# Kernel optimization log

Hardware: AMD Instinct MI355X
Metric: run time of the kernel (lower is better)

Reference implementation:

```python
import jax, jax.numpy as jnp
import numpy as np

N, CIN, T = 10000, 64, 64
COUT, K = 64, 3


def setup_inputs() -> dict:
    key = jax.random.key(0)
    k1, k2, k3 = jax.random.split(key, 3)
    x = jax.random.normal(k1, (N, CIN, T), dtype=jnp.float32)
    # torch Conv1d default init: uniform(-1/sqrt(fan_in), 1/sqrt(fan_in))
    bound = 1.0 / np.sqrt(CIN * K)
    weight = jax.random.uniform(k2, (2 * COUT, CIN, K), dtype=jnp.float32, minval=-bound, maxval=bound)
    bias = jax.random.uniform(k3, (2 * COUT,), dtype=jnp.float32, minval=-bound, maxval=bound)
    return {"x": x, "weight": weight, "bias": bias}


def reference(x, weight, bias):
    # Batched 1D conv over time for all nodes at once (equivalent to the
    # per-node loop in the original, since weights are shared).
    # x: [N, Cin, T], weight: [2*Cout, Cin, K] -> y: [N, 2*Cout, T-K+1]
    y = jax.lax.conv_general_dilated(
        x, weight, window_strides=(1,), padding="VALID",
        dimension_numbers=("NCH", "OIH", "NCH"))
    y = y + bias[None, :, None]
    # GLU along channel dim: first half gated by sigmoid of second half
    a, b = jnp.split(y, 2, axis=1)
    return a * jax.nn.sigmoid(b)
```

## Files before the change

kernel.cpp:

```cpp
#include <hip/hip_runtime.h>
#include <hip/hip_bf16.h>

typedef __attribute__((ext_vector_type(8))) short short8;
typedef __attribute__((ext_vector_type(4))) float float4v;

#define NSAMP 10000
#define CIN   64
#define TLEN  64
#define COUT  64
#define TOUT  62

static __device__ __forceinline__ ushort f2bf(float v) {
    unsigned int x = __float_as_uint(v);
    return (ushort)((x + 0x7fffu + ((x >> 16) & 1u)) >> 16);
}

__global__ void prep_weights(const float* __restrict__ w, ushort* __restrict__ wa) {
    int o = blockIdx.x * blockDim.x + threadIdx.x;
    if (o >= 128 * 192) return;
    int co = o / 192;
    int kk = o - co * 192;
    int k  = kk >> 6;
    int ci = kk & 63;
    wa[o] = f2bf(w[co * 192 + ci * 3 + k]);
}

__global__ __launch_bounds__(256, 2)
void conv_glu(const float* __restrict__ x, const ushort* __restrict__ wa,
              const float* __restrict__ bias, float* __restrict__ out) {
    const int n   = blockIdx.x;
    const int tid = threadIdx.x;
    const int w   = tid >> 6;
    const int L   = tid & 63;
    const int l   = L & 15;
    const int q   = L >> 4;
    const int h   = w & 1;
    const int nh  = w >> 1;
    const int t0base = nh * 32;

    const float* xs = x + n * (CIN * TLEN);

    short8 afr[4][6];
#pragma unroll
    for (int mt = 0; mt < 4; ++mt) {
        int co = 32 * h + 16 * (mt & 1) + 64 * (mt >> 1) + l;
        const short8* wrow = (const short8*)(wa + co * 192);
#pragma unroll
        for (int kc = 0; kc < 6; ++kc)
            afr[mt][kc] = wrow[kc * 4 + q];
    }

    float4v acc[4][2];
#pragma unroll
    for (int mt = 0; mt < 4; ++mt)
#pragma unroll
        for (int nt = 0; nt < 2; ++nt)
            acc[mt][nt] = (float4v){0.f, 0.f, 0.f, 0.f};

#pragma unroll
    for (int kc = 0; kc < 6; ++kc) {
        const int kcv = kc >> 1;
        const int cib = (kc & 1) * 32 + q * 8;
#pragma unroll
        for (int nt = 0; nt < 2; ++nt) {
            int t = t0base + nt * 16 + l + kcv;
            if (t > 63) t = 63;
            const float* p = xs + cib * TLEN + t;
            short8 bfr;
#pragma unroll
            for (int j = 0; j < 8; ++j)
                bfr[j] = (short)f2bf(p[j * TLEN]);
#pragma unroll
            for (int mt = 0; mt < 4; ++mt)
                acc[mt][nt] = __builtin_amdgcn_mfma_f32_16x16x32_bf16(
                    afr[mt][kc], bfr, acc[mt][nt], 0, 0, 0);
        }
    }

#pragma unroll
    for (int p2 = 0; p2 < 2; ++p2) {
#pragma unroll
        for (int nt = 0; nt < 2; ++nt) {
#pragma unroll
            for (int r = 0; r < 4; ++r) {
                int co = 32 * h + 16 * p2 + 4 * q + r;
                int t  = t0base + nt * 16 + l;
                float a = acc[p2][nt][r]     + bias[co];
                float g = acc[p2 + 2][nt][r] + bias[co + 64];
                float sg = 1.0f / (1.0f + __expf(-g));
                if (t < TOUT)
                    out[(n * COUT + co) * TOUT + t] = a * sg;
            }
        }
    }
}

extern "C" void kernel_launch(void* const* d_in, const int* in_sizes, int n_in,
                              void* d_out, int out_size, void* d_ws, size_t ws_size,
                              hipStream_t stream) {
    const float* x    = (const float*)d_in[0];
    const float* wt   = (const float*)d_in[1];
    const float* bias = (const float*)d_in[2];
    ushort*      wa   = (ushort*)d_ws;
    float*       out  = (float*)d_out;

    prep_weights<<<96, 256, 0, stream>>>(wt, wa);
    conv_glu<<<NSAMP, 256, 0, stream>>>(x, wa, bias, out);
}
```

Before: 403.7 us.

## Stage x in LDS as transposed swizzled bf16 and stream weight fragments

Each block loads its sample's x tile with coalesced float4 reads, converts pairs to bf16 with the packed convert instruction, and writes a time-major, XOR-swizzled layout into shared memory. MFMA B fragments then come from single 16-byte LDS reads instead of eight strided scalar global loads with software rounding. Weight fragments are loaded per k-chunk rather than all held in registers, and the occupancy hint is raised from 2 to 4 blocks per CU. This adds a barrier and 8KB of LDS per block, and the weights are now reloaded from cache inside the loop.

```diff
diff --git a/kernel.cpp b/kernel.cpp
--- a/kernel.cpp
+++ b/kernel.cpp
@@ -15,6 +15,12 @@
     return (ushort)((x + 0x7fffu + ((x >> 16) & 1u)) >> 16);
 }
 
+static __device__ __forceinline__ unsigned int cvt_pk_bf16(float a, float b) {
+    unsigned int r;
+    asm("v_cvt_pk_bf16_f32 %0, %1, %2" : "=v"(r) : "v"(a), "v"(b));
+    return r;
+}
+
 __global__ void prep_weights(const float* __restrict__ w, ushort* __restrict__ wa) {
     int o = blockIdx.x * blockDim.x + threadIdx.x;
     if (o >= 128 * 192) return;
@@ -25,9 +31,11 @@
     wa[o] = f2bf(w[co * 192 + ci * 3 + k]);
 }
 
-__global__ __launch_bounds__(256, 2)
+__global__ __launch_bounds__(256, 4)
 void conv_glu(const float* __restrict__ x, const ushort* __restrict__ wa,
               const float* __restrict__ bias, float* __restrict__ out) {
+    __shared__ __align__(16) ushort xT[64 * 64];
+
     const int n   = blockIdx.x;
     const int tid = threadIdx.x;
     const int w   = tid >> 6;
@@ -40,14 +48,31 @@
 
     const float* xs = x + n * (CIN * TLEN);
 
-    short8 afr[4][6];
+    {
+        const int cig = tid >> 4;
+        const int ts  = (tid & 15) * 4;
+        const float* p = xs + cig * 4 * TLEN + ts;
+        float4v v0 = *(const float4v*)(p);
+        float4v v1 = *(const float4v*)(p + TLEN);
+        float4v v2 = *(const float4v*)(p + 2 * TLEN);
+        float4v v3 = *(const float4v*)(p + 3 * TLEN);
+        char* base = (char*)xT;
+#pragma unroll
+        for (int r = 0; r < 4; ++r) {
+            int t = ts + r;
+            uint2 val;
+            val.x = cvt_pk_bf16(v0[r], v1[r]);
+            val.y = cvt_pk_bf16(v2[r], v3[r]);
+            *(uint2*)(base + t * 128 + ((cig * 8) ^ ((t & 7) << 4))) = val;
+        }
+    }
+    __syncthreads();
+
+    const ushort* arow[4];
 #pragma unroll
     for (int mt = 0; mt < 4; ++mt) {
         int co = 32 * h + 16 * (mt & 1) + 64 * (mt >> 1) + l;
-        const short8* wrow = (const short8*)(wa + co * 192);
-#pragma unroll
-        for (int kc = 0; kc < 6; ++kc)
-            afr[mt][kc] = wrow[kc * 4 + q];
+        arow[mt] = wa + co * 192 + q * 8;
     }
 
     float4v acc[4][2];
@@ -59,21 +84,23 @@
 
 #pragma unroll
     for (int kc = 0; kc < 6; ++kc) {
-        const int kcv = kc >> 1;
-        const int cib = (kc & 1) * 32 + q * 8;
+        short8 afr[4];
+#pragma unroll
+        for (int mt = 0; mt < 4; ++mt)
+            afr[mt] = *(const short8*)(arow[mt] + kc * 32);
+
+        const int tap  = kc >> 1;
+        const int cib2 = (kc & 1) * 64 + q * 16;
 #pragma unroll
         for (int nt = 0; nt < 2; ++nt) {
-            int t = t0base + nt * 16 + l + kcv;
+            int t = t0base + nt * 16 + l + tap;
             if (t > 63) t = 63;
-            const float* p = xs + cib * TLEN + t;
-            short8 bfr;
-#pragma unroll
-            for (int j = 0; j < 8; ++j)
-                bfr[j] = (short)f2bf(p[j * TLEN]);
+            const short8 bfr = *(const short8*)((const char*)xT + t * 128
+                                                + (cib2 ^ ((t & 7) << 4)));
 #pragma unroll
             for (int mt = 0; mt < 4; ++mt)
                 acc[mt][nt] = __builtin_amdgcn_mfma_f32_16x16x32_bf16(
-                    afr[mt][kc], bfr, acc[mt][nt], 0, 0, 0);
+                    afr[mt], bfr, acc[mt][nt], 0, 0, 0);
         }
     }
 
```

After: 361.1 us. 1.12x faster.

## Process four samples per block with prefetched loads and swizzled LDS staging

Applied to the files above, without the earlier changes.

Each block now handles four samples. It keeps the weight fragments and biases in registers and reuses them across samples, and it prefetches the global input two samples ahead in registers. The input is converted to bf16 with packed converts and written once into a double-buffered, XOR-swizzled LDS tile, replacing the redundant strided scalar global reads and conversions done per MFMA fragment. Outputs use nontemporal stores. The cost is more registers, a barrier per sample, and fewer blocks (2500), which may reduce occupancy and latency hiding.

```diff
diff --git a/kernel.cpp b/kernel.cpp
--- a/kernel.cpp
+++ b/kernel.cpp
@@ -3,16 +3,26 @@
 
 typedef __attribute__((ext_vector_type(8))) short short8;
 typedef __attribute__((ext_vector_type(4))) float float4v;
+typedef __attribute__((ext_vector_type(2))) float float2v;
+typedef __attribute__((ext_vector_type(4))) unsigned int uint4v;
 
 #define NSAMP 10000
 #define CIN   64
 #define TLEN  64
 #define COUT  64
 #define TOUT  62
+#define SPB   4
+#define NBLK  (NSAMP / SPB)
 
 static __device__ __forceinline__ ushort f2bf(float v) {
     unsigned int x = __float_as_uint(v);
     return (ushort)((x + 0x7fffu + ((x >> 16) & 1u)) >> 16);
+}
+
+static __device__ __forceinline__ unsigned int cvt_pk_bf16(float a, float b) {
+    unsigned int r;
+    asm("v_cvt_pk_bf16_f32 %0, %1, %2" : "=v"(r) : "v"(a), "v"(b));
+    return r;
 }
 
 __global__ void prep_weights(const float* __restrict__ w, ushort* __restrict__ wa) {
@@ -25,10 +35,17 @@
     wa[o] = f2bf(w[co * 192 + ci * 3 + k]);
 }
 
+static __device__ __forceinline__ void issue8(float2v (&dst)[8], const float* p) {
+#pragma unroll
+    for (int j = 0; j < 8; ++j)
+        dst[j] = *(const float2v*)(p + j * TLEN);
+}
+
 __global__ __launch_bounds__(256, 2)
 void conv_glu(const float* __restrict__ x, const ushort* __restrict__ wa,
               const float* __restrict__ bias, float* __restrict__ out) {
-    const int n   = blockIdx.x;
+    __shared__ __align__(16) ushort xT[2][64 * 64];
+
     const int tid = threadIdx.x;
     const int w   = tid >> 6;
     const int L   = tid & 63;
@@ -37,8 +54,11 @@
     const int h   = w & 1;
     const int nh  = w >> 1;
     const int t0base = nh * 32;
+    const int n0  = blockIdx.x * SPB;
 
-    const float* xs = x + n * (CIN * TLEN);
+    const int t2 = tid & 31;
+    const int c8 = tid >> 5;
+    const float* xs0 = x + (long)n0 * (CIN * TLEN) + c8 * 8 * TLEN + 2 * t2;
 
     short8 afr[4][6];
 #pragma unroll
@@ -50,48 +70,82 @@
             afr[mt][kc] = wrow[kc * 4 + q];
     }
 
-    float4v acc[4][2];
+    float bv[2][4], bg[2][4];
 #pragma unroll
-    for (int mt = 0; mt < 4; ++mt)
+    for (int p2 = 0; p2 < 2; ++p2)
 #pragma unroll
-        for (int nt = 0; nt < 2; ++nt)
-            acc[mt][nt] = (float4v){0.f, 0.f, 0.f, 0.f};
+        for (int r = 0; r < 4; ++r) {
+            int co = 32 * h + 16 * p2 + 4 * q + r;
+            bv[p2][r] = bias[co];
+            bg[p2][r] = bias[co + 64];
+        }
+
+    float2v ld[3][8];
+    issue8(ld[0], xs0);
+    issue8(ld[1], xs0 + CIN * TLEN);
 
 #pragma unroll
-    for (int kc = 0; kc < 6; ++kc) {
-        const int kcv = kc >> 1;
-        const int cib = (kc & 1) * 32 + q * 8;
+    for (int s = 0; s < SPB; ++s) {
+        if (s + 2 < SPB)
+            issue8(ld[(s + 2) % 3], xs0 + (long)(s + 2) * (CIN * TLEN));
+
+        {
+            char* base = (char*)xT[s & 1];
 #pragma unroll
-        for (int nt = 0; nt < 2; ++nt) {
-            int t = t0base + nt * 16 + l + kcv;
-            if (t > 63) t = 63;
-            const float* p = xs + cib * TLEN + t;
-            short8 bfr;
+            for (int r = 0; r < 2; ++r) {
+                int t = 2 * t2 + r;
+                uint4v val;
 #pragma unroll
-            for (int j = 0; j < 8; ++j)
-                bfr[j] = (short)f2bf(p[j * TLEN]);
-#pragma unroll
-            for (int mt = 0; mt < 4; ++mt)
-                acc[mt][nt] = __builtin_amdgcn_mfma_f32_16x16x32_bf16(
-                    afr[mt][kc], bfr, acc[mt][nt], 0, 0, 0);
-        }
-    }
-
-#pragma unroll
-    for (int p2 = 0; p2 < 2; ++p2) {
-#pragma unroll
-        for (int nt = 0; nt < 2; ++nt) {
-#pragma unroll
-            for (int r = 0; r < 4; ++r) {
-                int co = 32 * h + 16 * p2 + 4 * q + r;
-                int t  = t0base + nt * 16 + l;
-                float a = acc[p2][nt][r]     + bias[co];
-                float g = acc[p2 + 2][nt][r] + bias[co + 64];
-                float sg = 1.0f / (1.0f + __expf(-g));
-                if (t < TOUT)
-                    out[(n * COUT + co) * TOUT + t] = a * sg;
+                for (int k2 = 0; k2 < 4; ++k2)
+                    val[k2] = cvt_pk_bf16(ld[s % 3][2 * k2][r],
+                                          ld[s % 3][2 * k2 + 1][r]);
+                *(uint4v*)(base + t * 128 + ((c8 * 16) ^ ((t & 7) << 4))) = val;
             }
         }
+
+        asm volatile("s_waitcnt lgkmcnt(0)" ::: "memory");
+        __builtin_amdgcn_s_barrier();
+
+        float4v acc[4][2];
+#pragma unroll
+        for (int mt = 0; mt < 4; ++mt)
+#pragma unroll
+            for (int nt = 0; nt < 2; ++nt)
+                acc[mt][nt] = (float4v){0.f, 0.f, 0.f, 0.f};
+
+        const char* rbase = (const char*)xT[s & 1];
+#pragma unroll
+        for (int kc = 0; kc < 6; ++kc) {
+            const int tap  = kc >> 1;
+            const int cib2 = (kc & 1) * 64 + q * 16;
+#pragma unroll
+            for (int nt = 0; nt < 2; ++nt) {
+                int t = t0base + nt * 16 + l + tap;
+                if (t > 63) t = 63;
+                const short8 bfr = *(const short8*)(rbase + t * 128
+                                                    + (cib2 ^ ((t & 7) << 4)));
+#pragma unroll
+                for (int mt = 0; mt < 4; ++mt)
+                    acc[mt][nt] = __builtin_amdgcn_mfma_f32_16x16x32_bf16(
+                        afr[mt][kc], bfr, acc[mt][nt], 0, 0, 0);
+            }
+        }
+
+        float* outn = out + (long)(n0 + s) * (COUT * TOUT);
+#pragma unroll
+        for (int p2 = 0; p2 < 2; ++p2)
+#pragma unroll
+            for (int nt = 0; nt < 2; ++nt)
+#pragma unroll
+                for (int r = 0; r < 4; ++r) {
+                    int co = 32 * h + 16 * p2 + 4 * q + r;
+                    int t  = t0base + nt * 16 + l;
+                    float a = acc[p2][nt][r]     + bv[p2][r];
+                    float g = acc[p2 + 2][nt][r] + bg[p2][r];
+                    float sg = 1.0f / (1.0f + __expf(-g));
+                    if (t < TOUT)
+                        __builtin_nontemporal_store(a * sg, &outn[co * TOUT + t]);
+                }
     }
 }
 
@@ -105,5 +159,5 @@
     float*       out  = (float*)d_out;
 
     prep_weights<<<96, 256, 0, stream>>>(wt, wa);
-    conv_glu<<<NSAMP, 256, 0, stream>>>(x, wa, bias, out);
+    conv_glu<<<NBLK, 256, 0, stream>>>(x, wa, bias, out);
 }
```

New measurement: 366.8 us. 9.2% less time.
